# Kernel tuning notes

Measured on AMD Instinct MI355X. Metric: run time of the kernel, lower is better.

The kernel has to match this reference:

```python
import jax, jax.numpy as jnp
import numpy as np

B, T, C, H = 8, 2048, 768, 64

def setup_inputs() -> dict:
    key = jax.random.key(0)
    k1, k2, k3, k4 = jax.random.split(key, 4)
    x = jax.random.normal(k1, (B, T, C), dtype=jnp.float32)
    Wk = jax.random.normal(k2, (C, H), dtype=jnp.float32) * 0.02
    Wq = jax.random.normal(k3, (C, H), dtype=jnp.float32) * 0.02
    Wv = jax.random.normal(k4, (C, H), dtype=jnp.float32) * 0.02
    return {"x": x, "Wk": Wk, "Wq": Wq, "Wv": Wv}

def reference(x, Wk, Wq, Wv):
    # QKV projections (no bias): [B,T,C] @ [C,H] -> [B,T,H]
    k = jnp.einsum('btc,ch->bth', x, Wk)
    q = jnp.einsum('btc,ch->bth', x, Wq)
    v = jnp.einsum('btc,ch->bth', x, Wv)
    scale = 1.0 / jnp.sqrt(jnp.asarray(q.shape[-1], q.dtype))
    # scores: [B,T,T]
    wei = jnp.einsum('bth,bsh->bts', q, k) * scale
    # causal mask: upper triangle (k=1) set to -inf before softmax
    causal = jnp.tril(jnp.ones((wei.shape[1], wei.shape[2]), dtype=bool))
    wei = jnp.where(causal[None, :, :], wei, -jnp.inf)
    wei = jax.nn.softmax(wei, axis=-1)
    # dropout deterministic (training=False) -> identity
    out = jnp.einsum('bts,bsh->bth', wei, v)
    return out
```

## Files before the change

kernel.cpp:

```cpp
#include <hip/hip_runtime.h>
#include <hip/hip_bf16.h>
#include <stdint.h>

#define BB 8
#define TT 2048
#define CC 768
#define NTPB 72

typedef __bf16 bf16x8 __attribute__((ext_vector_type(8)));
typedef float f32x4 __attribute__((ext_vector_type(4)));
typedef float f32x16 __attribute__((ext_vector_type(16)));

__device__ inline __bf16 f2b(float f) {
    __hip_bfloat16 h = __float2bfloat16(f);
    return __builtin_bit_cast(__bf16, h);
}
__device__ inline ushort f2bits(float f) {
    __hip_bfloat16 h = __float2bfloat16(f);
    return __builtin_bit_cast(ushort, h);
}
__device__ inline float bits2f(ushort u) {
    return __builtin_bit_cast(float, ((uint32_t)u) << 16);
}
__device__ inline uint32_t cvtpk(float lo, float hi) {
    uint32_t r;
    asm("v_cvt_pk_bf16_f32 %0, %1, %2" : "=v"(r) : "v"(lo), "v"(hi));
    return r;
}
__device__ inline void pswap(uint32_t& a, uint32_t& b) {
    asm volatile("v_permlane32_swap_b32 %0, %1" : "+v"(a), "+v"(b));
}

#define GLL16(gp, lp)                                                          \
    __builtin_amdgcn_global_load_lds(                                          \
        (const __attribute__((address_space(1))) unsigned int*)(gp),           \
        (__attribute__((address_space(3))) unsigned int*)(lp), 16, 0, 0)

__launch_bounds__(256)
__global__ void wt_kernel(const float* __restrict__ Wk, const float* __restrict__ Wq,
                          const float* __restrict__ Wv, ushort* __restrict__ WtF) {
    __shared__ float tile[64][65];
    int m  = blockIdx.x / 12;
    int c0 = (blockIdx.x % 12) * 64;
    const float* W = (m == 0) ? Wq : ((m == 1) ? Wk : Wv);
    int tid = threadIdx.x;
#pragma unroll
    for (int i = 0; i < 4; i++) {
        int r   = (tid >> 4) + i * 16;
        int col = (tid & 15) * 4;
        float4 v = *(const float4*)&W[(size_t)(c0 + r) * 64 + col];
        tile[r][col] = v.x; tile[r][col + 1] = v.y;
        tile[r][col + 2] = v.z; tile[r][col + 3] = v.w;
    }
    __syncthreads();
    int j  = tid >> 2;
    int cc = (tid & 3) * 16;
    ushort tmp[16];
#pragma unroll
    for (int e = 0; e < 16; e++) tmp[e] = f2bits(tile[cc + e][j]);
    int c  = m * 64 + j;
    int kb = c0 + cc;
    int kc = kb >> 5;
    int h4 = (kb >> 3) & 3;
    ushort* dst = &WtF[((size_t)kc * 192 + c) * 32 + h4 * 8];
    *(uint4*)(dst)     = *(uint4*)&tmp[0];
    *(uint4*)(dst + 8) = *(uint4*)&tmp[8];
}

__launch_bounds__(256, 2)
__global__ void qkv_kernel(const float* __restrict__ x, const ushort* __restrict__ WtF,
                           ushort* __restrict__ qws, ushort* __restrict__ kws,
                           ushort* __restrict__ vws) {
    __shared__ float  xsA[4][32 * 32];
    __shared__ ushort xsB[4][6144];

    int tid  = threadIdx.x;
    int wid  = tid >> 6;
    int lane = tid & 63;
    int l15  = lane & 15;
    int hi4  = lane >> 4;
    int row0 = blockIdx.x * 32;

    int rA  = tid >> 3;
    int gcA = (tid & 7) ^ (rA & 7);
    const float* gpA = x + (size_t)(row0 + rA) * CC + gcA * 4;

    int PB0 = tid, PB1 = tid + 256, PB2 = tid + 512;
    int LB0 = PB0 ^ ((PB0 >> 3) & 3);
    int LB1 = PB1 ^ ((PB1 >> 3) & 3);
    int LB2 = PB2 ^ ((PB2 >> 3) & 3);

    int PrB[3];
#pragma unroll
    for (int nt = 0; nt < 3; nt++) {
        int Lr = (wid * 48 + nt * 16 + l15) * 4 + hi4;
        PrB[nt] = Lr ^ ((Lr >> 3) & 3);
    }

    f32x4 acc[2][3];
#pragma unroll
    for (int mm = 0; mm < 2; mm++)
#pragma unroll
        for (int nt = 0; nt < 3; nt++) acc[mm][nt] = (f32x4){0.f, 0.f, 0.f, 0.f};

    auto stage = [&](int t) {
        int buf = t & 3;
        GLL16(gpA + t * 32, &xsA[buf][(size_t)tid * 4]);
        const ushort* bsrc = WtF + (size_t)t * 6144;
        GLL16(bsrc + LB0 * 8, &xsB[buf][PB0 * 8]);
        GLL16(bsrc + LB1 * 8, &xsB[buf][PB1 * 8]);
        GLL16(bsrc + LB2 * 8, &xsB[buf][PB2 * 8]);
    };

    stage(0); stage(1); stage(2); stage(3);

#pragma unroll
    for (int t = 0; t < 24; t++) {
        if (t <= 20)      asm volatile("s_waitcnt vmcnt(12)" ::: "memory");
        else if (t == 21) asm volatile("s_waitcnt vmcnt(8)" ::: "memory");
        else if (t == 22) asm volatile("s_waitcnt vmcnt(4)" ::: "memory");
        else              asm volatile("s_waitcnt vmcnt(0)" ::: "memory");
        __builtin_amdgcn_s_barrier();
        __builtin_amdgcn_sched_barrier(0);

        int buf = t & 3;
        bf16x8 af[2];
#pragma unroll
        for (int mm = 0; mm < 2; mm++) {
            int row = mm * 16 + l15;
            const float* base = &xsA[buf][row * 32];
            float4 fa = *(const float4*)(base + (((2 * hi4)     ^ (row & 7)) * 4));
            float4 fb = *(const float4*)(base + (((2 * hi4 + 1) ^ (row & 7)) * 4));
            uint32_t w0 = cvtpk(fa.x, fa.y), w1 = cvtpk(fa.z, fa.w);
            uint32_t w2 = cvtpk(fb.x, fb.y), w3 = cvtpk(fb.z, fb.w);
            uint4 u = {w0, w1, w2, w3};
            af[mm] = __builtin_bit_cast(bf16x8, u);
        }
#pragma unroll
        for (int nt = 0; nt < 3; nt++) {
            bf16x8 b = __builtin_bit_cast(bf16x8, *(const uint4*)&xsB[buf][PrB[nt] * 8]);
            acc[0][nt] = __builtin_amdgcn_mfma_f32_16x16x32_bf16(af[0], b, acc[0][nt], 0, 0, 0);
            acc[1][nt] = __builtin_amdgcn_mfma_f32_16x16x32_bf16(af[1], b, acc[1][nt], 0, 0, 0);
        }
        __builtin_amdgcn_s_barrier();
        if (t + 4 < 24) stage(t + 4);
    }

    const float qscale = 0.125f * 1.4426950408889634f;
    int bidx = row0 >> 11;
#pragma unroll
    for (int mm = 0; mm < 2; mm++) {
        int r0 = row0 + mm * 16 + 4 * hi4;
        int t0 = r0 & 2047;
#pragma unroll
        for (int nt = 0; nt < 3; nt++) {
            int c = wid * 48 + nt * 16 + l15;
            int m = c >> 6;
            int j = c & 63;
            if (m == 0) {
#pragma unroll
                for (int r = 0; r < 4; r++)
                    qws[(size_t)(r0 + r) * 64 + j] = f2bits(acc[mm][nt][r] * qscale);
            } else if (m == 1) {
#pragma unroll
                for (int r = 0; r < 4; r++)
                    kws[(size_t)(r0 + r) * 64 + j] = f2bits(acc[mm][nt][r]);
            } else {
                ushort4 pk;
                pk.x = f2bits(acc[mm][nt][0]);
                pk.y = f2bits(acc[mm][nt][1]);
                pk.z = f2bits(acc[mm][nt][2]);
                pk.w = f2bits(acc[mm][nt][3]);
                *(ushort4*)&vws[((size_t)bidx * 64 + j) * TT + t0] = pk;
            }
        }
    }
}

__launch_bounds__(256, 3)
__global__ void flash_kernel(const ushort* __restrict__ qg, const ushort* __restrict__ kg,
                             const ushort* __restrict__ vtg, float* __restrict__ out,
                             ushort* __restrict__ pO, float* __restrict__ pM,
                             float* __restrict__ pL) {
    __shared__ ushort Ks[3][64 * 64];
    __shared__ ushort Vs[3][64 * 64];

    int tid  = threadIdx.x;
    int wid  = tid >> 6;
    int lane = tid & 63;
    int l31  = lane & 31;
    int hi   = lane >> 5;

    int b  = blockIdx.x / NTPB;
    int tp = blockIdx.x - b * NTPB;
    int g  = 0;
    while (tp >= ((g + 2) * (g + 2)) >> 2) g++;
    int seg   = tp - (((g + 1) * (g + 1)) >> 2);
    int nseg  = (g + 2) >> 1;
    int Qb    = g * 128;
    int Q0w   = Qb + wid * 32;
    int s_beg = seg * 256;
    int s_end = (s_beg + 256 < Qb + 128) ? s_beg + 256 : Qb + 128;
    int nt    = (s_end - s_beg) >> 6;

    int rS  = tid >> 3;
    int gcS = (tid & 7) ^ (rS & 7);
    const ushort* kS = kg  + ((size_t)b * TT + rS) * 64 + gcS * 8;
    const ushort* vS = vtg + ((size_t)b * 64 + rS) * TT + gcS * 8;

    auto stage = [&](int tt) {
        int buf = tt % 3;
        int ss  = s_beg + tt * 64;
        const ushort* kA = kS + (size_t)ss * 64;
        const ushort* vA = vS + ss;
        GLL16(kA,            &Ks[buf][tid * 8]);
        GLL16(kA + 32 * 64,  &Ks[buf][(tid + 256) * 8]);
        GLL16(vA,            &Vs[buf][tid * 8]);
        GLL16(vA + 32 * TT,  &Vs[buf][(tid + 256) * 8]);
    };

    const ushort* qp = qg + ((size_t)b * TT + Q0w + l31) * 64 + hi * 8;
    bf16x8 qf[4];
#pragma unroll
    for (int c = 0; c < 4; c++)
        qf[c] = __builtin_bit_cast(bf16x8, *(const uint4*)(qp + c * 16));

    f32x16 o0 = (f32x16)(0.f), o1 = (f32x16)(0.f);
    float m  = -INFINITY;
    float lp = 0.f;

    stage(0);
    if (nt > 1) stage(1);

    for (int t = 0; t < nt; t++) {
        if (t < nt - 1) asm volatile("s_waitcnt vmcnt(4)" ::: "memory");
        else            asm volatile("s_waitcnt vmcnt(0)" ::: "memory");
        __builtin_amdgcn_s_barrier();
        __builtin_amdgcn_sched_barrier(0);
        if (t + 2 < nt) stage(t + 2);

        int s0 = s_beg + t * 64;
        if (s0 < Q0w + 32) {
            int buf = t % 3;
            bf16x8 kf[2][4];
#pragma unroll
            for (int tt = 0; tt < 2; tt++) {
                int rk = tt * 32 + l31;
                const ushort* base = &Ks[buf][rk * 64];
                int sw = rk & 7;
#pragma unroll
                for (int c = 0; c < 4; c++)
                    kf[tt][c] = __builtin_bit_cast(bf16x8,
                        *(const uint4*)(base + (((c * 2 + hi) ^ sw) * 8)));
            }

            f32x16 st0 = (f32x16)(0.f), st1 = (f32x16)(0.f);
            __builtin_amdgcn_s_setprio(1);
#pragma unroll
            for (int c = 0; c < 4; c++)
                st0 = __builtin_amdgcn_mfma_f32_32x32x16_bf16(kf[0][c], qf[c], st0, 0, 0, 0);
#pragma unroll
            for (int c = 0; c < 4; c++)
                st1 = __builtin_amdgcn_mfma_f32_32x32x16_bf16(kf[1][c], qf[c], st1, 0, 0, 0);
            __builtin_amdgcn_s_setprio(0);

            if (s0 + 63 > Q0w) {
                int th0 = Q0w + l31 - s0 - 4 * hi;
                int th1 = th0 - 32;
#pragma unroll
                for (int r = 0; r < 16; r++) {
                    int kvl = (r & 3) + 8 * (r >> 2);
                    if (kvl > th0) st0[r] = -INFINITY;
                    if (kvl > th1) st1[r] = -INFINITY;
                }
            }

            float a[16];
#pragma unroll
            for (int r = 0; r < 16; r++) a[r] = fmaxf(st0[r], st1[r]);
#pragma unroll
            for (int off = 8; off > 0; off >>= 1)
#pragma unroll
                for (int i = 0; i < 8; i++)
                    if (i < off) a[i] = fmaxf(a[i], a[i + off]);
            float pmax = fmaxf(a[0], __shfl_xor(a[0], 32));
            if (__any(pmax > m + 11.54f)) {
                float mn = fmaxf(m, pmax);
                float al = exp2f(m - mn);
                lp *= al;
#pragma unroll
                for (int r = 0; r < 16; r++) { o0[r] *= al; o1[r] *= al; }
                m = mn;
            }
#pragma unroll
            for (int r = 0; r < 16; r++) {
                st0[r] = exp2f(st0[r] - m);
                st1[r] = exp2f(st1[r] - m);
            }
            float s[16];
#pragma unroll
            for (int r = 0; r < 16; r++) s[r] = st0[r] + st1[r];
#pragma unroll
            for (int off = 8; off > 0; off >>= 1)
#pragma unroll
                for (int i = 0; i < 8; i++)
                    if (i < off) s[i] += s[i + off];
            lp += s[0];

            bf16x8 pf[4];
            {
                uint32_t w0, w1, w2, w3;
                w0 = cvtpk(st0[0], st0[1]);  w1 = cvtpk(st0[2], st0[3]);
                w2 = cvtpk(st0[4], st0[5]);  w3 = cvtpk(st0[6], st0[7]);
                pswap(w0, w2); pswap(w1, w3);
                uint4 u0 = {w0, w1, w2, w3}; pf[0] = __builtin_bit_cast(bf16x8, u0);
                w0 = cvtpk(st0[8], st0[9]);  w1 = cvtpk(st0[10], st0[11]);
                w2 = cvtpk(st0[12], st0[13]); w3 = cvtpk(st0[14], st0[15]);
                pswap(w0, w2); pswap(w1, w3);
                uint4 u1 = {w0, w1, w2, w3}; pf[1] = __builtin_bit_cast(bf16x8, u1);
                w0 = cvtpk(st1[0], st1[1]);  w1 = cvtpk(st1[2], st1[3]);
                w2 = cvtpk(st1[4], st1[5]);  w3 = cvtpk(st1[6], st1[7]);
                pswap(w0, w2); pswap(w1, w3);
                uint4 u2 = {w0, w1, w2, w3}; pf[2] = __builtin_bit_cast(bf16x8, u2);
                w0 = cvtpk(st1[8], st1[9]);  w1 = cvtpk(st1[10], st1[11]);
                w2 = cvtpk(st1[12], st1[13]); w3 = cvtpk(st1[14], st1[15]);
                pswap(w0, w2); pswap(w1, w3);
                uint4 u3 = {w0, w1, w2, w3}; pf[3] = __builtin_bit_cast(bf16x8, u3);
            }

            bf16x8 vf[2][4];
#pragma unroll
            for (int ht = 0; ht < 2; ht++) {
                int rv = ht * 32 + l31;
                const ushort* base = &Vs[buf][rv * 64];
                int sw = rv & 7;
#pragma unroll
                for (int c = 0; c < 4; c++)
                    vf[ht][c] = __builtin_bit_cast(bf16x8,
                        *(const uint4*)(base + (((c * 2 + hi) ^ sw) * 8)));
            }

            __builtin_amdgcn_s_setprio(1);
#pragma unroll
            for (int c = 0; c < 4; c++)
                o0 = __builtin_amdgcn_mfma_f32_32x32x16_bf16(vf[0][c], pf[c], o0, 0, 0, 0);
#pragma unroll
            for (int c = 0; c < 4; c++)
                o1 = __builtin_amdgcn_mfma_f32_32x32x16_bf16(vf[1][c], pf[c], o1, 0, 0, 0);
            __builtin_amdgcn_s_setprio(0);
        }
    }

    float lsum = lp + __shfl_xor(lp, 32);

    if (nseg == 1) {
        float inv = 1.f / lsum;
        float* ob = out + ((size_t)b * TT + Q0w + l31) * 64;
#pragma unroll
        for (int gg = 0; gg < 4; gg++) {
            float4 v0 = {o0[4*gg] * inv, o0[4*gg+1] * inv, o0[4*gg+2] * inv, o0[4*gg+3] * inv};
            *(float4*)(ob + 8 * gg + 4 * hi) = v0;
            float4 v1 = {o1[4*gg] * inv, o1[4*gg+1] * inv, o1[4*gg+2] * inv, o1[4*gg+3] * inv};
            *(float4*)(ob + 32 + 8 * gg + 4 * hi) = v1;
        }
    } else {
        int tb = b * NTPB + tp;
        ushort* pb = pO + (size_t)tb * 8192 + (size_t)(wid * 32 + l31) * 64;
#pragma unroll
        for (int gg = 0; gg < 4; gg++) {
            ushort4 v0 = {f2bits(o0[4*gg]), f2bits(o0[4*gg+1]),
                          f2bits(o0[4*gg+2]), f2bits(o0[4*gg+3])};
            *(ushort4*)(pb + 8 * gg + 4 * hi) = v0;
            ushort4 v1 = {f2bits(o1[4*gg]), f2bits(o1[4*gg+1]),
                          f2bits(o1[4*gg+2]), f2bits(o1[4*gg+3])};
            *(ushort4*)(pb + 32 + 8 * gg + 4 * hi) = v1;
        }
        if (hi == 0) {
            pM[(size_t)tb * 128 + wid * 32 + l31] = m;
            pL[(size_t)tb * 128 + wid * 32 + l31] = lsum;
        }
    }
}

__launch_bounds__(256)
__global__ void merge_kernel(const ushort* __restrict__ pO, const float* __restrict__ pM,
                             const float* __restrict__ pL, float* __restrict__ out) {
    int b    = blockIdx.x / 14;
    int g    = 2 + (blockIdx.x % 14);
    int nseg = (g + 2) >> 1;
    int tbase = b * NTPB + (((g + 1) * (g + 1)) >> 2);

    int row = threadIdx.x >> 1;
    int hh  = (threadIdx.x & 1) * 32;

    float mstar = -INFINITY;
    for (int s = 0; s < nseg; s++)
        mstar = fmaxf(mstar, pM[(size_t)(tbase + s) * 128 + row]);

    float oa[32];
#pragma unroll
    for (int i = 0; i < 32; i++) oa[i] = 0.f;
    float la = 0.f;
    for (int s = 0; s < nseg; s++) {
        float w = exp2f(pM[(size_t)(tbase + s) * 128 + row] - mstar);
        la += w * pL[(size_t)(tbase + s) * 128 + row];
        const ushort* pp = pO + (size_t)(tbase + s) * 8192 + (size_t)row * 64 + hh;
        uint4 u0 = *(const uint4*)(pp);
        uint4 u1 = *(const uint4*)(pp + 8);
        uint4 u2 = *(const uint4*)(pp + 16);
        uint4 u3 = *(const uint4*)(pp + 24);
        const uint4 uu[4] = {u0, u1, u2, u3};
#pragma unroll
        for (int q = 0; q < 4; q++) {
#pragma unroll
            for (int e = 0; e < 4; e++) {
                uint32_t wdw = ((const uint32_t*)&uu[q])[e];
                oa[q*8 + e*2]     += w * bits2f((ushort)(wdw & 0xffff));
                oa[q*8 + e*2 + 1] += w * bits2f((ushort)(wdw >> 16));
            }
        }
    }
    float inv = 1.f / la;
    float* ob = out + ((size_t)b * TT + g * 128 + row) * 64 + hh;
#pragma unroll
    for (int i = 0; i < 8; i++) {
        float4 v = {oa[i*4] * inv, oa[i*4+1] * inv, oa[i*4+2] * inv, oa[i*4+3] * inv};
        *(float4*)(ob + i * 4) = v;
    }
}

extern "C" void kernel_launch(void* const* d_in, const int* in_sizes, int n_in,
                              void* d_out, int out_size, void* d_ws, size_t ws_size,
                              hipStream_t stream) {
    const float* x  = (const float*)d_in[0];
    const float* Wk = (const float*)d_in[1];
    const float* Wq = (const float*)d_in[2];
    const float* Wv = (const float*)d_in[3];
    float* out = (float*)d_out;

    char* ws = (char*)d_ws;
    ushort* WtF = (ushort*)(ws);
    ushort* qws = (ushort*)(ws + 0x50000);
    ushort* kws = (ushort*)(ws + 0x250000);
    ushort* vws = (ushort*)(ws + 0x450000);
    ushort* pO  = (ushort*)(ws + 0x650000);
    float*  pM  = (float*)(ws + 0x1050000);
    float*  pL  = (float*)(ws + 0x1098000);

    wt_kernel<<<36, 256, 0, stream>>>(Wk, Wq, Wv, WtF);
    qkv_kernel<<<(BB * TT) / 32, 256, 0, stream>>>(x, WtF, qws, kws, vws);
    flash_kernel<<<BB * NTPB, 256, 0, stream>>>(qws, kws, vws, out, pO, pM, pL);
    merge_kernel<<<BB * 14, 256, 0, stream>>>(pO, pM, pL, out);
}
```

Baseline: 53.52 us.

## Fuse split-KV merge into flash kernel via last-block atomic counter

Removes the separate merge kernel. Each split-KV block publishes its partial output, max and sum, fences, and increments a per-(batch, query-group) counter. The last block to arrive performs the merge. Counters are zeroed in the weight-transpose kernel. Block indexing also changes to interleave batches (b = blockIdx & 7), which spreads work from different query groups across the launch. This saves a kernel launch and its tail, at the cost of atomics and fences, plus a serial merge tail on the last-arriving block.

New measurement: 137.8 us. 157% more time.

```diff
diff --git a/kernel.cpp b/kernel.cpp
--- a/kernel.cpp
+++ b/kernel.cpp
@@ -38,7 +38,10 @@
 
 __launch_bounds__(256)
 __global__ void wt_kernel(const float* __restrict__ Wk, const float* __restrict__ Wq,
-                          const float* __restrict__ Wv, ushort* __restrict__ WtF) {
+                          const float* __restrict__ Wv, ushort* __restrict__ WtF,
+                          unsigned int* __restrict__ cnt) {
+    if (blockIdx.x == 0 && threadIdx.x < BB * 14)
+        cnt[threadIdx.x] = 0;
     __shared__ float tile[64][65];
     int m  = blockIdx.x / 12;
     int c0 = (blockIdx.x % 12) * 64;
@@ -181,9 +184,10 @@
 __global__ void flash_kernel(const ushort* __restrict__ qg, const ushort* __restrict__ kg,
                              const ushort* __restrict__ vtg, float* __restrict__ out,
                              ushort* __restrict__ pO, float* __restrict__ pM,
-                             float* __restrict__ pL) {
+                             float* __restrict__ pL, unsigned int* __restrict__ cnt) {
     __shared__ ushort Ks[3][64 * 64];
     __shared__ ushort Vs[3][64 * 64];
+    __shared__ int lastFlag;
 
     int tid  = threadIdx.x;
     int wid  = tid >> 6;
@@ -191,8 +195,8 @@
     int l31  = lane & 31;
     int hi   = lane >> 5;
 
-    int b  = blockIdx.x / NTPB;
-    int tp = blockIdx.x - b * NTPB;
+    int b  = blockIdx.x & 7;
+    int tp = blockIdx.x >> 3;
     int g  = 0;
     while (tp >= ((g + 2) * (g + 2)) >> 2) g++;
     int seg   = tp - (((g + 1) * (g + 1)) >> 2);
@@ -363,35 +367,37 @@
             float4 v1 = {o1[4*gg] * inv, o1[4*gg+1] * inv, o1[4*gg+2] * inv, o1[4*gg+3] * inv};
             *(float4*)(ob + 32 + 8 * gg + 4 * hi) = v1;
         }
-    } else {
-        int tb = b * NTPB + tp;
-        ushort* pb = pO + (size_t)tb * 8192 + (size_t)(wid * 32 + l31) * 64;
-#pragma unroll
-        for (int gg = 0; gg < 4; gg++) {
-            ushort4 v0 = {f2bits(o0[4*gg]), f2bits(o0[4*gg+1]),
-                          f2bits(o0[4*gg+2]), f2bits(o0[4*gg+3])};
-            *(ushort4*)(pb + 8 * gg + 4 * hi) = v0;
-            ushort4 v1 = {f2bits(o1[4*gg]), f2bits(o1[4*gg+1]),
-                          f2bits(o1[4*gg+2]), f2bits(o1[4*gg+3])};
-            *(ushort4*)(pb + 32 + 8 * gg + 4 * hi) = v1;
-        }
-        if (hi == 0) {
-            pM[(size_t)tb * 128 + wid * 32 + l31] = m;
-            pL[(size_t)tb * 128 + wid * 32 + l31] = lsum;
-        }
-    }
-}
-
-__launch_bounds__(256)
-__global__ void merge_kernel(const ushort* __restrict__ pO, const float* __restrict__ pM,
-                             const float* __restrict__ pL, float* __restrict__ out) {
-    int b    = blockIdx.x / 14;
-    int g    = 2 + (blockIdx.x % 14);
-    int nseg = (g + 2) >> 1;
+        return;
+    }
+
+    int tb = b * NTPB + tp;
+    ushort* pb = pO + (size_t)tb * 8192 + (size_t)(wid * 32 + l31) * 64;
+#pragma unroll
+    for (int gg = 0; gg < 4; gg++) {
+        ushort4 v0 = {f2bits(o0[4*gg]), f2bits(o0[4*gg+1]),
+                      f2bits(o0[4*gg+2]), f2bits(o0[4*gg+3])};
+        *(ushort4*)(pb + 8 * gg + 4 * hi) = v0;
+        ushort4 v1 = {f2bits(o1[4*gg]), f2bits(o1[4*gg+1]),
+                      f2bits(o1[4*gg+2]), f2bits(o1[4*gg+3])};
+        *(ushort4*)(pb + 32 + 8 * gg + 4 * hi) = v1;
+    }
+    if (hi == 0) {
+        pM[(size_t)tb * 128 + wid * 32 + l31] = m;
+        pL[(size_t)tb * 128 + wid * 32 + l31] = lsum;
+    }
+
+    __threadfence();
+    if (tid == 0) {
+        unsigned int old = atomicAdd(&cnt[b * 14 + (g - 2)], 1u);
+        lastFlag = (old == (unsigned int)(nseg - 1));
+    }
+    __syncthreads();
+    if (!lastFlag) return;
+    __threadfence();
+
     int tbase = b * NTPB + (((g + 1) * (g + 1)) >> 2);
-
-    int row = threadIdx.x >> 1;
-    int hh  = (threadIdx.x & 1) * 32;
+    int row = tid >> 1;
+    int hh  = (tid & 1) * 32;
 
     float mstar = -INFINITY;
     for (int s = 0; s < nseg; s++)
@@ -446,9 +452,9 @@
     ushort* pO  = (ushort*)(ws + 0x650000);
     float*  pM  = (float*)(ws + 0x1050000);
     float*  pL  = (float*)(ws + 0x1098000);
-
-    wt_kernel<<<36, 256, 0, stream>>>(Wk, Wq, Wv, WtF);
+    unsigned int* cnt = (unsigned int*)(ws + 0x10E0000);
+
+    wt_kernel<<<36, 256, 0, stream>>>(Wk, Wq, Wv, WtF, cnt);
     qkv_kernel<<<(BB * TT) / 32, 256, 0, stream>>>(x, WtF, qws, kws, vws);
-    flash_kernel<<<BB * NTPB, 256, 0, stream>>>(qws, kws, vws, out, pO, pM, pL);
-    merge_kernel<<<BB * 14, 256, 0, stream>>>(pO, pM, pL, out);
-}
+    flash_kernel<<<BB * NTPB, 256, 0, stream>>>(qws, kws, vws, out, pO, pM, pL, cnt);
+}
```
